# Optimization experiments

Measured on AMD Instinct MI355X. Metric: run time of the kernel, lower is better.

The kernel has to match this reference:

```python
import jax, jax.numpy as jnp
import numpy as np

N, DEG, F = 500000, 16, 128
H1, H2, OUT = 256, 256, 128


def setup_inputs() -> dict:
    key = jax.random.key(0)
    ks = jax.random.split(key, 8)
    s = lambda fan_in: 1.0 / np.sqrt(fan_in)
    return {
        "message": jax.random.normal(ks[0], (N, DEG, F), dtype=jnp.float32),
        "features": jax.random.normal(ks[1], (N, F), dtype=jnp.float32),
        "global_features": jax.random.normal(ks[2], (N, F), dtype=jnp.float32),
        "W1": jax.random.normal(ks[3], (3 * F, H1), dtype=jnp.float32) * s(3 * F),
        "b1": jnp.zeros((H1,), dtype=jnp.float32),
        "W2": jax.random.normal(ks[4], (H1, H2), dtype=jnp.float32) * s(H1),
        "b2": jnp.zeros((H2,), dtype=jnp.float32),
        "W3": jax.random.normal(ks[5], (H2, OUT), dtype=jnp.float32) * s(H2),
        "b3": jnp.zeros((OUT,), dtype=jnp.float32),
    }


def reference(message, features, global_features, W1, b1, W2, b2, W3, b3):
    # mailbox sum-aggregate over neighbors: [N, deg, F] -> [N, F]
    agg = jnp.sum(message, axis=1)
    # concat aggregated messages with node + global features: [N, 3F]
    x = jnp.concatenate([agg, features, global_features], axis=1)
    # MLP: Linear+ReLU, Linear+ReLU, Linear
    h = jax.nn.relu(x @ W1 + b1)
    h = jax.nn.relu(h @ W2 + b2)
    out = h @ W3 + b3
    # row-wise L2 (Frobenius over dim=1) normalization
    norm = jnp.linalg.norm(out, axis=1, keepdims=True)
    return out / (norm + 1e-8)
```

## Files before the change

### kernel.cpp

```cpp
#include <hip/hip_runtime.h>


typedef short short8   __attribute__((ext_vector_type(8)));
typedef short short4_t __attribute__((ext_vector_type(4)));
typedef float f32x4    __attribute__((ext_vector_type(4)));

#define SWZ(row, off) ((off) ^ (((row) & 7) << 4))

__device__ __forceinline__ unsigned short f2bf(float f) {
    unsigned int u = __float_as_uint(f);
    u += 0x7fffu + ((u >> 16) & 1u);
    return (unsigned short)(u >> 16);
}

__global__ void prep_weights(const float* __restrict__ W1,
                             const float* __restrict__ W2,
                             const float* __restrict__ W3,
                             short* __restrict__ pw1,
                             short* __restrict__ pw2,
                             short* __restrict__ pw3) {
    int idx = blockIdx.x * 256 + threadIdx.x;
    if (idx < 98304) {
        int j = idx & 7, l = (idx >> 3) & 63, g = idx >> 9;
        int ks = g % 12, tn = g / 12;
        int n = tn * 16 + (l & 15);
        int k = ks * 32 + ((l >> 4) << 3) + j;
        pw1[idx] = (short)f2bf(W1[k * 256 + n]);
    } else if (idx < 98304 + 65536) {
        int e = idx - 98304;
        int j = e & 7, l = (e >> 3) & 63, g = e >> 9;
        int ks = g & 7, tn = g >> 3;
        int n = tn * 16 + (l & 15);
        int k = ks * 32 + ((l >> 4) << 3) + j;
        pw2[e] = (short)f2bf(W2[k * 256 + n]);
    } else if (idx < 98304 + 65536 + 32768) {
        int e = idx - 98304 - 65536;
        int j = e & 7, l = (e >> 3) & 63, g = e >> 9;
        int ks = g & 7, tn = g >> 3;
        int n = tn * 16 + (l & 15);
        int k = ks * 32 + ((l >> 4) << 3) + j;
        pw3[e] = (short)f2bf(W3[k * 128 + n]);
    }
}

__global__ __launch_bounds__(256, 4) void node_net_fused(
    const float* __restrict__ msg,
    const float* __restrict__ feat,
    const float* __restrict__ glob,
    const float* __restrict__ b1v,
    const float* __restrict__ b2v,
    const float* __restrict__ b3v,
    const short* __restrict__ pw1,
    const short* __restrict__ pw2,
    const short* __restrict__ pw3,
    float* __restrict__ out,
    int n_rows)
{
    __shared__ char lds[32768];
    char* regA = lds;
    char* regB = lds + 16384;

    {
        const unsigned key = ((unsigned)blockIdx.x * 2654435761u) >> 30;
        const int spin = (int)key * 500;
        for (int i = 0; i < spin; ++i)
            asm volatile("s_nop 0" ::: "memory");
    }

    const int tid  = threadIdx.x;
    const int lane = tid & 63;
    const int w    = tid >> 6;
    const int lr   = lane & 15;
    const int lk   = lane >> 4;
    const long long r0 = (long long)blockIdx.x * 32;

    const f32x4 zero4 = {0.f, 0.f, 0.f, 0.f};

    f32x4 fr[4], gr[4];
    #pragma unroll
    for (int q = 0; q < 4; ++q) {
        int r = (tid >> 5) + q * 8;
        long long row = r0 + r;
        fr[q] = zero4; gr[q] = zero4;
        if (row < n_rows) {
            fr[q] = __builtin_nontemporal_load((const f32x4*)feat + row * 32 + (tid & 31));
            gr[q] = __builtin_nontemporal_load((const f32x4*)glob + row * 32 + (tid & 31));
        }
    }

    #pragma unroll 1
    for (int pp = 0; pp < 4; ++pp) {
        const int rA = 8 * w + 2 * pp;
        const long long rowA = r0 + rA;
        const f32x4* base = (const f32x4*)msg + rowA * 512;
        f32x4 tA[8], tB[8];
        const bool okA = rowA < n_rows;
        const bool okB = (rowA + 1) < n_rows;
        #pragma unroll
        for (int i = 0; i < 8; ++i)
            tA[i] = okA ? __builtin_nontemporal_load(base + i * 64 + lane) : zero4;
        #pragma unroll
        for (int i = 0; i < 8; ++i)
            tB[i] = okB ? __builtin_nontemporal_load(base + 512 + i * 64 + lane) : zero4;
        f32x4 sA = ((tA[0]+tA[1])+(tA[2]+tA[3])) + ((tA[4]+tA[5])+(tA[6]+tA[7]));
        f32x4 sB = ((tB[0]+tB[1])+(tB[2]+tB[3])) + ((tB[4]+tB[5])+(tB[6]+tB[7]));
        #pragma unroll
        for (int c = 0; c < 4; ++c) {
            sA[c] += __shfl_xor(sA[c], 32);
            sB[c] += __shfl_xor(sB[c], 32);
        }
        f32x4 s = (lane < 32) ? sA : sB;
        short4_t s4;
        s4[0] = (short)f2bf(s[0]); s4[1] = (short)f2bf(s[1]);
        s4[2] = (short)f2bf(s[2]); s4[3] = (short)f2bf(s[3]);
        const int orow = rA + (lane >> 5);
        *(short4_t*)(regB + SWZ(orow, orow * 256 + (lane & 31) * 8)) = s4;
    }
    __syncthreads();

    #pragma unroll
    for (int q = 0; q < 4; ++q) {
        int r = (tid >> 5) + q * 8;
        short4_t s4;
        s4[0] = (short)f2bf(fr[q][0]); s4[1] = (short)f2bf(fr[q][1]);
        s4[2] = (short)f2bf(fr[q][2]); s4[3] = (short)f2bf(fr[q][3]);
        *(short4_t*)(regA + SWZ(r, r * 256 + (tid & 31) * 8)) = s4;
    }

    f32x4 acc1[2][4];
    #pragma unroll
    for (int ri = 0; ri < 2; ++ri)
        #pragma unroll
        for (int ci = 0; ci < 4; ++ci) acc1[ri][ci] = zero4;

    #pragma unroll
    for (int s = 0; s < 4; ++s) {
        short8 a[2], b[4];
        #pragma unroll
        for (int ri = 0; ri < 2; ++ri) {
            int row = ri * 16 + lr;
            a[ri] = *(const short8*)(regB + SWZ(row, row * 256 + s * 64 + lk * 16));
        }
        #pragma unroll
        for (int ci = 0; ci < 4; ++ci) {
            int tn = w * 4 + ci;
            b[ci] = *(const short8*)(pw1 + (((tn * 12 + s) * 64 + lane) << 3));
        }
        #pragma unroll
        for (int ri = 0; ri < 2; ++ri)
            #pragma unroll
            for (int ci = 0; ci < 4; ++ci)
                acc1[ri][ci] = __builtin_amdgcn_mfma_f32_16x16x32_bf16(
                    a[ri], b[ci], acc1[ri][ci], 0, 0, 0);
    }
    __syncthreads();

    #pragma unroll
    for (int q = 0; q < 4; ++q) {
        int r = (tid >> 5) + q * 8;
        short4_t s4;
        s4[0] = (short)f2bf(gr[q][0]); s4[1] = (short)f2bf(gr[q][1]);
        s4[2] = (short)f2bf(gr[q][2]); s4[3] = (short)f2bf(gr[q][3]);
        *(short4_t*)(regB + 8192 + SWZ(r, r * 256 + (tid & 31) * 8)) = s4;
    }

    #pragma unroll
    for (int s = 0; s < 4; ++s) {
        short8 a[2], b[4];
        #pragma unroll
        for (int ri = 0; ri < 2; ++ri) {
            int row = ri * 16 + lr;
            a[ri] = *(const short8*)(regA + SWZ(row, row * 256 + s * 64 + lk * 16));
        }
        #pragma unroll
        for (int ci = 0; ci < 4; ++ci) {
            int tn = w * 4 + ci;
            b[ci] = *(const short8*)(pw1 + (((tn * 12 + 4 + s) * 64 + lane) << 3));
        }
        #pragma unroll
        for (int ri = 0; ri < 2; ++ri)
            #pragma unroll
            for (int ci = 0; ci < 4; ++ci)
                acc1[ri][ci] = __builtin_amdgcn_mfma_f32_16x16x32_bf16(
                    a[ri], b[ci], acc1[ri][ci], 0, 0, 0);
    }
    __syncthreads();

    #pragma unroll
    for (int s = 0; s < 4; ++s) {
        short8 a[2], b[4];
        #pragma unroll
        for (int ri = 0; ri < 2; ++ri) {
            int row = ri * 16 + lr;
            a[ri] = *(const short8*)(regB + 8192 + SWZ(row, row * 256 + s * 64 + lk * 16));
        }
        #pragma unroll
        for (int ci = 0; ci < 4; ++ci) {
            int tn = w * 4 + ci;
            b[ci] = *(const short8*)(pw1 + (((tn * 12 + 8 + s) * 64 + lane) << 3));
        }
        #pragma unroll
        for (int ri = 0; ri < 2; ++ri)
            #pragma unroll
            for (int ci = 0; ci < 4; ++ci)
                acc1[ri][ci] = __builtin_amdgcn_mfma_f32_16x16x32_bf16(
                    a[ri], b[ci], acc1[ri][ci], 0, 0, 0);
    }

    #pragma unroll
    for (int ci = 0; ci < 4; ++ci) {
        int col = w * 64 + ci * 16 + lr;
        float bias = b1v[col];
        #pragma unroll
        for (int ri = 0; ri < 2; ++ri)
            #pragma unroll
            for (int i = 0; i < 4; ++i) {
                int row = ri * 16 + lk * 4 + i;
                float v = fmaxf(acc1[ri][ci][i] + bias, 0.f);
                *(short*)(regA + SWZ(row, row * 512 + col * 2)) = (short)f2bf(v);
            }
    }
    __syncthreads();

    f32x4 acc2[2][4];
    #pragma unroll
    for (int ri = 0; ri < 2; ++ri)
        #pragma unroll
        for (int ci = 0; ci < 4; ++ci) acc2[ri][ci] = zero4;

    #pragma unroll
    for (int s = 0; s < 8; ++s) {
        short8 a[2], b[4];
        #pragma unroll
        for (int ri = 0; ri < 2; ++ri) {
            int row = ri * 16 + lr;
            a[ri] = *(const short8*)(regA + SWZ(row, row * 512 + s * 64 + lk * 16));
        }
        #pragma unroll
        for (int ci = 0; ci < 4; ++ci) {
            int tn = w * 4 + ci;
            b[ci] = *(const short8*)(pw2 + (((tn * 8 + s) * 64 + lane) << 3));
        }
        #pragma unroll
        for (int ri = 0; ri < 2; ++ri)
            #pragma unroll
            for (int ci = 0; ci < 4; ++ci)
                acc2[ri][ci] = __builtin_amdgcn_mfma_f32_16x16x32_bf16(
                    a[ri], b[ci], acc2[ri][ci], 0, 0, 0);
    }

    #pragma unroll
    for (int ci = 0; ci < 4; ++ci) {
        int col = w * 64 + ci * 16 + lr;
        float bias = b2v[col];
        #pragma unroll
        for (int ri = 0; ri < 2; ++ri)
            #pragma unroll
            for (int i = 0; i < 4; ++i) {
                int row = ri * 16 + lk * 4 + i;
                float v = fmaxf(acc2[ri][ci][i] + bias, 0.f);
                *(short*)(regB + SWZ(row, row * 512 + col * 2)) = (short)f2bf(v);
            }
    }
    __syncthreads();

    f32x4 acc3[2][2];
    #pragma unroll
    for (int ri = 0; ri < 2; ++ri)
        #pragma unroll
        for (int ci = 0; ci < 2; ++ci) acc3[ri][ci] = zero4;

    #pragma unroll
    for (int s = 0; s < 8; ++s) {
        short8 a[2], b[2];
        #pragma unroll
        for (int ri = 0; ri < 2; ++ri) {
            int row = ri * 16 + lr;
            a[ri] = *(const short8*)(regB + SWZ(row, row * 512 + s * 64 + lk * 16));
        }
        #pragma unroll
        for (int ci = 0; ci < 2; ++ci) {
            int tn = w * 2 + ci;
            b[ci] = *(const short8*)(pw3 + (((tn * 8 + s) * 64 + lane) << 3));
        }
        #pragma unroll
        for (int ri = 0; ri < 2; ++ri)
            #pragma unroll
            for (int ci = 0; ci < 2; ++ci)
                acc3[ri][ci] = __builtin_amdgcn_mfma_f32_16x16x32_bf16(
                    a[ri], b[ci], acc3[ri][ci], 0, 0, 0);
    }

    #pragma unroll
    for (int ci = 0; ci < 2; ++ci) {
        int col = w * 32 + ci * 16 + lr;
        float bias = b3v[col];
        #pragma unroll
        for (int ri = 0; ri < 2; ++ri)
            #pragma unroll
            for (int i = 0; i < 4; ++i) {
                int row = ri * 16 + lk * 4 + i;
                float v = acc3[ri][ci][i] + bias;
                *(float*)(regA + SWZ(row, row * 512 + col * 4)) = v;
            }
    }
    __syncthreads();

    #pragma unroll
    for (int pass = 0; pass < 4; ++pass) {
        const int r  = (tid >> 5) + pass * 8;
        const int fl = tid & 31;
        f32x4 v = *(const f32x4*)(regA + SWZ(r, r * 512 + fl * 16));
        float ss = v[0]*v[0] + v[1]*v[1] + v[2]*v[2] + v[3]*v[3];
        ss += __shfl_xor(ss, 1, 32);
        ss += __shfl_xor(ss, 2, 32);
        ss += __shfl_xor(ss, 4, 32);
        ss += __shfl_xor(ss, 8, 32);
        ss += __shfl_xor(ss, 16, 32);
        float inv = 1.f / (sqrtf(ss) + 1e-8f);
        long long row = r0 + r;
        if (row < n_rows) {
            f32x4 o = v * inv;
            __builtin_nontemporal_store(o, (f32x4*)out + row * 32 + fl);
        }
    }
}

extern "C" void kernel_launch(void* const* d_in, const int* in_sizes, int n_in,
                              void* d_out, int out_size, void* d_ws, size_t ws_size,
                              hipStream_t stream) {
    const float* msg  = (const float*)d_in[0];
    const float* feat = (const float*)d_in[1];
    const float* glob = (const float*)d_in[2];
    const float* W1   = (const float*)d_in[3];
    const float* b1   = (const float*)d_in[4];
    const float* W2   = (const float*)d_in[5];
    const float* b2   = (const float*)d_in[6];
    const float* W3   = (const float*)d_in[7];
    const float* b3   = (const float*)d_in[8];
    float* out = (float*)d_out;

    const int n_rows = in_sizes[1] / 128;

    short* pw1 = (short*)d_ws;
    short* pw2 = pw1 + 98304;
    short* pw3 = pw2 + 65536;

    hipLaunchKernelGGL(prep_weights, dim3(768), dim3(256), 0, stream,
                       W1, W2, W3, pw1, pw2, pw3);

    const int nblocks = (n_rows + 31) / 32;
    hipLaunchKernelGGL(node_net_fused, dim3(nblocks), dim3(256), 0, stream,
                       msg, feat, glob, b1, b2, b3, pw1, pw2, pw3, out, n_rows);
}
```

Measured before the change: 1.119 ms.

## Process two 32-row tiles per block, prefetching second tile's messages during MLP

Each block now handles 64 rows as two 32-row tiles. The message loads for the second tile are spread across the first tile's MLP stages in register buffers, so HBM reads overlap MFMA work. Feature and global inputs are staged into LDS together, so layer 1 runs as one 12-step K loop with fewer barriers. The staggered-start spin loop is removed. LDS grows to 48KB, launch bounds drop to 3 blocks per CU, and the extra prefetch registers raise register pressure.

```diff
diff --git a/kernel.cpp b/kernel.cpp
--- a/kernel.cpp
+++ b/kernel.cpp
@@ -43,7 +43,7 @@
     }
 }
 
-__global__ __launch_bounds__(256, 4) void node_net_fused(
+__global__ __launch_bounds__(256, 3) void node_net_fused2(
     const float* __restrict__ msg,
     const float* __restrict__ feat,
     const float* __restrict__ glob,
@@ -56,27 +56,48 @@
     float* __restrict__ out,
     int n_rows)
 {
-    __shared__ char lds[32768];
-    char* regA = lds;
-    char* regB = lds + 16384;
-
-    {
-        const unsigned key = ((unsigned)blockIdx.x * 2654435761u) >> 30;
-        const int spin = (int)key * 500;
-        for (int i = 0; i < spin; ++i)
-            asm volatile("s_nop 0" ::: "memory");
-    }
+    __shared__ char lds[49152];
+    char* XA = lds;
+    char* H  = lds + 24576;
+    char* AB = lds + 40960;
 
     const int tid  = threadIdx.x;
     const int lane = tid & 63;
     const int w    = tid >> 6;
     const int lr   = lane & 15;
     const int lk   = lane >> 4;
-    const long long r0 = (long long)blockIdx.x * 32;
-
+    const long long r0 = (long long)blockIdx.x * 64;
     const f32x4 zero4 = {0.f, 0.f, 0.f, 0.f};
 
     f32x4 fr[4], gr[4];
+    f32x4 cA[8], cB[8];
+
+#define ISSUE_PAIR(k) {                                                        \
+    const long long gA_ = r0 + 32 + 8 * w + 2 * (k);                           \
+    const f32x4* base_ = (const f32x4*)msg + gA_ * 512;                        \
+    const bool okA_ = gA_ < n_rows, okB_ = (gA_ + 1) < n_rows;                 \
+    _Pragma("unroll")                                                          \
+    for (int i = 0; i < 8; ++i)                                                \
+        cA[i] = okA_ ? __builtin_nontemporal_load(base_ + i * 64 + lane) : zero4; \
+    _Pragma("unroll")                                                          \
+    for (int i = 0; i < 8; ++i)                                                \
+        cB[i] = okB_ ? __builtin_nontemporal_load(base_ + 512 + i * 64 + lane) : zero4; }
+
+#define CONSUME_PAIR(k) {                                                      \
+    f32x4 sA_ = ((cA[0]+cA[1])+(cA[2]+cA[3])) + ((cA[4]+cA[5])+(cA[6]+cA[7])); \
+    f32x4 sB_ = ((cB[0]+cB[1])+(cB[2]+cB[3])) + ((cB[4]+cB[5])+(cB[6]+cB[7])); \
+    _Pragma("unroll")                                                          \
+    for (int c = 0; c < 4; ++c) {                                              \
+        sA_[c] += __shfl_xor(sA_[c], 32);                                      \
+        sB_[c] += __shfl_xor(sB_[c], 32);                                      \
+    }                                                                          \
+    f32x4 s_ = (lane < 32) ? sA_ : sB_;                                        \
+    short4_t s4_;                                                              \
+    s4_[0]=(short)f2bf(s_[0]); s4_[1]=(short)f2bf(s_[1]);                      \
+    s4_[2]=(short)f2bf(s_[2]); s4_[3]=(short)f2bf(s_[3]);                      \
+    const int rb_ = 8 * w + 2 * (k) + (lane >> 5);                             \
+    *(short4_t*)(AB + SWZ(rb_, rb_ * 256 + (lane & 31) * 8)) = s4_; }
+
     #pragma unroll
     for (int q = 0; q < 4; ++q) {
         int r = (tid >> 5) + q * 8;
@@ -111,41 +132,42 @@
         }
         f32x4 s = (lane < 32) ? sA : sB;
         short4_t s4;
-        s4[0] = (short)f2bf(s[0]); s4[1] = (short)f2bf(s[1]);
-        s4[2] = (short)f2bf(s[2]); s4[3] = (short)f2bf(s[3]);
+        s4[0]=(short)f2bf(s[0]); s4[1]=(short)f2bf(s[1]);
+        s4[2]=(short)f2bf(s[2]); s4[3]=(short)f2bf(s[3]);
         const int orow = rA + (lane >> 5);
-        *(short4_t*)(regB + SWZ(orow, orow * 256 + (lane & 31) * 8)) = s4;
-    }
-    __syncthreads();
-
+        *(short4_t*)(XA + SWZ(orow, orow * 256 + (lane & 31) * 8)) = s4;
+    }
     #pragma unroll
     for (int q = 0; q < 4; ++q) {
         int r = (tid >> 5) + q * 8;
-        short4_t s4;
-        s4[0] = (short)f2bf(fr[q][0]); s4[1] = (short)f2bf(fr[q][1]);
-        s4[2] = (short)f2bf(fr[q][2]); s4[3] = (short)f2bf(fr[q][3]);
-        *(short4_t*)(regA + SWZ(r, r * 256 + (tid & 31) * 8)) = s4;
-    }
-
+        short4_t sf, sg;
+        sf[0]=(short)f2bf(fr[q][0]); sf[1]=(short)f2bf(fr[q][1]);
+        sf[2]=(short)f2bf(fr[q][2]); sf[3]=(short)f2bf(fr[q][3]);
+        sg[0]=(short)f2bf(gr[q][0]); sg[1]=(short)f2bf(gr[q][1]);
+        sg[2]=(short)f2bf(gr[q][2]); sg[3]=(short)f2bf(gr[q][3]);
+        *(short4_t*)(XA + 8192  + SWZ(r, r * 256 + (tid & 31) * 8)) = sf;
+        *(short4_t*)(XA + 16384 + SWZ(r, r * 256 + (tid & 31) * 8)) = sg;
+    }
+    __syncthreads();
+
+    ISSUE_PAIR(0)
     f32x4 acc1[2][4];
     #pragma unroll
     for (int ri = 0; ri < 2; ++ri)
         #pragma unroll
         for (int ci = 0; ci < 4; ++ci) acc1[ri][ci] = zero4;
-
-    #pragma unroll
-    for (int s = 0; s < 4; ++s) {
+    #pragma unroll
+    for (int ks = 0; ks < 12; ++ks) {
+        const int p = ks >> 2, s = ks & 3;
         short8 a[2], b[4];
         #pragma unroll
         for (int ri = 0; ri < 2; ++ri) {
             int row = ri * 16 + lr;
-            a[ri] = *(const short8*)(regB + SWZ(row, row * 256 + s * 64 + lk * 16));
-        }
-        #pragma unroll
-        for (int ci = 0; ci < 4; ++ci) {
-            int tn = w * 4 + ci;
-            b[ci] = *(const short8*)(pw1 + (((tn * 12 + s) * 64 + lane) << 3));
-        }
+            a[ri] = *(const short8*)(XA + p * 8192 + SWZ(row, row * 256 + s * 64 + lk * 16));
+        }
+        #pragma unroll
+        for (int ci = 0; ci < 4; ++ci)
+            b[ci] = *(const short8*)(pw1 + ((((w * 4 + ci) * 12 + ks) * 64 + lane) << 3));
         #pragma unroll
         for (int ri = 0; ri < 2; ++ri)
             #pragma unroll
@@ -153,60 +175,6 @@
                 acc1[ri][ci] = __builtin_amdgcn_mfma_f32_16x16x32_bf16(
                     a[ri], b[ci], acc1[ri][ci], 0, 0, 0);
     }
-    __syncthreads();
-
-    #pragma unroll
-    for (int q = 0; q < 4; ++q) {
-        int r = (tid >> 5) + q * 8;
-        short4_t s4;
-        s4[0] = (short)f2bf(gr[q][0]); s4[1] = (short)f2bf(gr[q][1]);
-        s4[2] = (short)f2bf(gr[q][2]); s4[3] = (short)f2bf(gr[q][3]);
-        *(short4_t*)(regB + 8192 + SWZ(r, r * 256 + (tid & 31) * 8)) = s4;
-    }
-
-    #pragma unroll
-    for (int s = 0; s < 4; ++s) {
-        short8 a[2], b[4];
-        #pragma unroll
-        for (int ri = 0; ri < 2; ++ri) {
-            int row = ri * 16 + lr;
-            a[ri] = *(const short8*)(regA + SWZ(row, row * 256 + s * 64 + lk * 16));
-        }
-        #pragma unroll
-        for (int ci = 0; ci < 4; ++ci) {
-            int tn = w * 4 + ci;
-            b[ci] = *(const short8*)(pw1 + (((tn * 12 + 4 + s) * 64 + lane) << 3));
-        }
-        #pragma unroll
-        for (int ri = 0; ri < 2; ++ri)
-            #pragma unroll
-            for (int ci = 0; ci < 4; ++ci)
-                acc1[ri][ci] = __builtin_amdgcn_mfma_f32_16x16x32_bf16(
-                    a[ri], b[ci], acc1[ri][ci], 0, 0, 0);
-    }
-    __syncthreads();
-
-    #pragma unroll
-    for (int s = 0; s < 4; ++s) {
-        short8 a[2], b[4];
-        #pragma unroll
-        for (int ri = 0; ri < 2; ++ri) {
-            int row = ri * 16 + lr;
-            a[ri] = *(const short8*)(regB + 8192 + SWZ(row, row * 256 + s * 64 + lk * 16));
-        }
-        #pragma unroll
-        for (int ci = 0; ci < 4; ++ci) {
-            int tn = w * 4 + ci;
-            b[ci] = *(const short8*)(pw1 + (((tn * 12 + 8 + s) * 64 + lane) << 3));
-        }
-        #pragma unroll
-        for (int ri = 0; ri < 2; ++ri)
-            #pragma unroll
-            for (int ci = 0; ci < 4; ++ci)
-                acc1[ri][ci] = __builtin_amdgcn_mfma_f32_16x16x32_bf16(
-                    a[ri], b[ci], acc1[ri][ci], 0, 0, 0);
-    }
-
     #pragma unroll
     for (int ci = 0; ci < 4; ++ci) {
         int col = w * 64 + ci * 16 + lr;
@@ -217,100 +185,112 @@
             for (int i = 0; i < 4; ++i) {
                 int row = ri * 16 + lk * 4 + i;
                 float v = fmaxf(acc1[ri][ci][i] + bias, 0.f);
-                *(short*)(regA + SWZ(row, row * 512 + col * 2)) = (short)f2bf(v);
-            }
-    }
-    __syncthreads();
-
-    f32x4 acc2[2][4];
-    #pragma unroll
-    for (int ri = 0; ri < 2; ++ri)
-        #pragma unroll
-        for (int ci = 0; ci < 4; ++ci) acc2[ri][ci] = zero4;
-
-    #pragma unroll
-    for (int s = 0; s < 8; ++s) {
-        short8 a[2], b[4];
-        #pragma unroll
-        for (int ri = 0; ri < 2; ++ri) {
-            int row = ri * 16 + lr;
-            a[ri] = *(const short8*)(regA + SWZ(row, row * 512 + s * 64 + lk * 16));
+                *(short*)(H + SWZ(row, row * 512 + col * 2)) = (short)f2bf(v);
+            }
+    }
+    __syncthreads();
+
+    CONSUME_PAIR(0)
+    ISSUE_PAIR(1)
+    {
+        f32x4 acc2[2][4];
+        #pragma unroll
+        for (int ri = 0; ri < 2; ++ri)
+            #pragma unroll
+            for (int ci = 0; ci < 4; ++ci) acc2[ri][ci] = zero4;
+        #pragma unroll
+        for (int s = 0; s < 8; ++s) {
+            short8 a[2], b[4];
+            #pragma unroll
+            for (int ri = 0; ri < 2; ++ri) {
+                int row = ri * 16 + lr;
+                a[ri] = *(const short8*)(H + SWZ(row, row * 512 + s * 64 + lk * 16));
+            }
+            #pragma unroll
+            for (int ci = 0; ci < 4; ++ci)
+                b[ci] = *(const short8*)(pw2 + ((((w * 4 + ci) * 8 + s) * 64 + lane) << 3));
+            #pragma unroll
+            for (int ri = 0; ri < 2; ++ri)
+                #pragma unroll
+                for (int ci = 0; ci < 4; ++ci)
+                    acc2[ri][ci] = __builtin_amdgcn_mfma_f32_16x16x32_bf16(
+                        a[ri], b[ci], acc2[ri][ci], 0, 0, 0);
         }
         #pragma unroll
         for (int ci = 0; ci < 4; ++ci) {
-            int tn = w * 4 + ci;
-            b[ci] = *(const short8*)(pw2 + (((tn * 8 + s) * 64 + lane) << 3));
-        }
-        #pragma unroll
-        for (int ri = 0; ri < 2; ++ri)
-            #pragma unroll
-            for (int ci = 0; ci < 4; ++ci)
-                acc2[ri][ci] = __builtin_amdgcn_mfma_f32_16x16x32_bf16(
-                    a[ri], b[ci], acc2[ri][ci], 0, 0, 0);
-    }
-
-    #pragma unroll
-    for (int ci = 0; ci < 4; ++ci) {
-        int col = w * 64 + ci * 16 + lr;
-        float bias = b2v[col];
-        #pragma unroll
-        for (int ri = 0; ri < 2; ++ri)
-            #pragma unroll
-            for (int i = 0; i < 4; ++i) {
-                int row = ri * 16 + lk * 4 + i;
-                float v = fmaxf(acc2[ri][ci][i] + bias, 0.f);
-                *(short*)(regB + SWZ(row, row * 512 + col * 2)) = (short)f2bf(v);
-            }
-    }
-    __syncthreads();
-
-    f32x4 acc3[2][2];
-    #pragma unroll
-    for (int ri = 0; ri < 2; ++ri)
-        #pragma unroll
-        for (int ci = 0; ci < 2; ++ci) acc3[ri][ci] = zero4;
-
-    #pragma unroll
-    for (int s = 0; s < 8; ++s) {
-        short8 a[2], b[2];
-        #pragma unroll
-        for (int ri = 0; ri < 2; ++ri) {
-            int row = ri * 16 + lr;
-            a[ri] = *(const short8*)(regB + SWZ(row, row * 512 + s * 64 + lk * 16));
+            int col = w * 64 + ci * 16 + lr;
+            float bias = b2v[col];
+            #pragma unroll
+            for (int ri = 0; ri < 2; ++ri)
+                #pragma unroll
+                for (int i = 0; i < 4; ++i) {
+                    int row = ri * 16 + lk * 4 + i;
+                    float v = fmaxf(acc2[ri][ci][i] + bias, 0.f);
+                    *(short*)(XA + SWZ(row, row * 512 + col * 2)) = (short)f2bf(v);
+                }
+        }
+    }
+    __syncthreads();
+
+    CONSUME_PAIR(1)
+    ISSUE_PAIR(2)
+    {
+        f32x4 acc3[2][2];
+        #pragma unroll
+        for (int ri = 0; ri < 2; ++ri)
+            #pragma unroll
+            for (int ci = 0; ci < 2; ++ci) acc3[ri][ci] = zero4;
+        #pragma unroll
+        for (int s = 0; s < 8; ++s) {
+            short8 a[2], b[2];
+            #pragma unroll
+            for (int ri = 0; ri < 2; ++ri) {
+                int row = ri * 16 + lr;
+                a[ri] = *(const short8*)(XA + SWZ(row, row * 512 + s * 64 + lk * 16));
+            }
+            #pragma unroll
+            for (int ci = 0; ci < 2; ++ci)
+                b[ci] = *(const short8*)(pw3 + ((((w * 2 + ci) * 8 + s) * 64 + lane) << 3));
+            #pragma unroll
+            for (int ri = 0; ri < 2; ++ri)
+                #pragma unroll
+                for (int ci = 0; ci < 2; ++ci)
+                    acc3[ri][ci] = __builtin_amdgcn_mfma_f32_16x16x32_bf16(
+                        a[ri], b[ci], acc3[ri][ci], 0, 0, 0);
         }
         #pragma unroll
         for (int ci = 0; ci < 2; ++ci) {
-            int tn = w * 2 + ci;
-            b[ci] = *(const short8*)(pw3 + (((tn * 8 + s) * 64 + lane) << 3));
-        }
-        #pragma unroll
-        for (int ri = 0; ri < 2; ++ri)
-            #pragma unroll
-            for (int ci = 0; ci < 2; ++ci)
-                acc3[ri][ci] = __builtin_amdgcn_mfma_f32_16x16x32_bf16(
-                    a[ri], b[ci], acc3[ri][ci], 0, 0, 0);
-    }
-
-    #pragma unroll
-    for (int ci = 0; ci < 2; ++ci) {
-        int col = w * 32 + ci * 16 + lr;
-        float bias = b3v[col];
-        #pragma unroll
-        for (int ri = 0; ri < 2; ++ri)
-            #pragma unroll
-            for (int i = 0; i < 4; ++i) {
-                int row = ri * 16 + lk * 4 + i;
-                float v = acc3[ri][ci][i] + bias;
-                *(float*)(regA + SWZ(row, row * 512 + col * 4)) = v;
-            }
-    }
-    __syncthreads();
-
+            int col = w * 32 + ci * 16 + lr;
+            float bias = b3v[col];
+            #pragma unroll
+            for (int ri = 0; ri < 2; ++ri)
+                #pragma unroll
+                for (int i = 0; i < 4; ++i) {
+                    int row = ri * 16 + lk * 4 + i;
+                    float v = acc3[ri][ci][i] + bias;
+                    *(float*)(H + SWZ(row, row * 512 + col * 4)) = v;
+                }
+        }
+    }
+    __syncthreads();
+
+    CONSUME_PAIR(2)
+    ISSUE_PAIR(3)
+    #pragma unroll
+    for (int q = 0; q < 4; ++q) {
+        int r = (tid >> 5) + q * 8;
+        long long row = r0 + 32 + r;
+        fr[q] = zero4; gr[q] = zero4;
+        if (row < n_rows) {
+            fr[q] = __builtin_nontemporal_load((const f32x4*)feat + row * 32 + (tid & 31));
+            gr[q] = __builtin_nontemporal_load((const f32x4*)glob + row * 32 + (tid & 31));
+        }
+    }
     #pragma unroll
     for (int pass = 0; pass < 4; ++pass) {
         const int r  = (tid >> 5) + pass * 8;
         const int fl = tid & 31;
-        f32x4 v = *(const f32x4*)(regA + SWZ(r, r * 512 + fl * 16));
+        f32x4 v = *(const f32x4*)(H + SWZ(r, r * 512 + fl * 16));
         float ss = v[0]*v[0] + v[1]*v[1] + v[2]*v[2] + v[3]*v[3];
         ss += __shfl_xor(ss, 1, 32);
         ss += __shfl_xor(ss, 2, 32);
@@ -324,6 +304,161 @@
             __builtin_nontemporal_store(o, (f32x4*)out + row * 32 + fl);
         }
     }
+    __syncthreads();
+
+    CONSUME_PAIR(3)
+    #pragma unroll
+    for (int q = 0; q < 4; ++q) {
+        int r = (tid >> 5) + q * 8;
+        short4_t sf, sg;
+        sf[0]=(short)f2bf(fr[q][0]); sf[1]=(short)f2bf(fr[q][1]);
+        sf[2]=(short)f2bf(fr[q][2]); sf[3]=(short)f2bf(fr[q][3]);
+        sg[0]=(short)f2bf(gr[q][0]); sg[1]=(short)f2bf(gr[q][1]);
+        sg[2]=(short)f2bf(gr[q][2]); sg[3]=(short)f2bf(gr[q][3]);
+        *(short4_t*)(XA + 8192  + SWZ(r, r * 256 + (tid & 31) * 8)) = sf;
+        *(short4_t*)(XA + 16384 + SWZ(r, r * 256 + (tid & 31) * 8)) = sg;
+    }
+    __syncthreads();
+
+    #pragma unroll
+    for (int ri = 0; ri < 2; ++ri)
+        #pragma unroll
+        for (int ci = 0; ci < 4; ++ci) acc1[ri][ci] = zero4;
+    #pragma unroll
+    for (int ks = 0; ks < 12; ++ks) {
+        const int p = ks >> 2, s = ks & 3;
+        const char* abase = (p == 0) ? AB : (XA + p * 8192);
+        short8 a[2], b[4];
+        #pragma unroll
+        for (int ri = 0; ri < 2; ++ri) {
+            int row = ri * 16 + lr;
+            a[ri] = *(const short8*)(abase + SWZ(row, row * 256 + s * 64 + lk * 16));
+        }
+        #pragma unroll
+        for (int ci = 0; ci < 4; ++ci)
+            b[ci] = *(const short8*)(pw1 + ((((w * 4 + ci) * 12 + ks) * 64 + lane) << 3));
+        #pragma unroll
+        for (int ri = 0; ri < 2; ++ri)
+            #pragma unroll
+            for (int ci = 0; ci < 4; ++ci)
+                acc1[ri][ci] = __builtin_amdgcn_mfma_f32_16x16x32_bf16(
+                    a[ri], b[ci], acc1[ri][ci], 0, 0, 0);
+    }
+    #pragma unroll
+    for (int ci = 0; ci < 4; ++ci) {
+        int col = w * 64 + ci * 16 + lr;
+        float bias = b1v[col];
+        #pragma unroll
+        for (int ri = 0; ri < 2; ++ri)
+            #pragma unroll
+            for (int i = 0; i < 4; ++i) {
+                int row = ri * 16 + lk * 4 + i;
+                float v = fmaxf(acc1[ri][ci][i] + bias, 0.f);
+                *(short*)(H + SWZ(row, row * 512 + col * 2)) = (short)f2bf(v);
+            }
+    }
+    __syncthreads();
+
+    {
+        f32x4 acc2[2][4];
+        #pragma unroll
+        for (int ri = 0; ri < 2; ++ri)
+            #pragma unroll
+            for (int ci = 0; ci < 4; ++ci) acc2[ri][ci] = zero4;
+        #pragma unroll
+        for (int s = 0; s < 8; ++s) {
+            short8 a[2], b[4];
+            #pragma unroll
+            for (int ri = 0; ri < 2; ++ri) {
+                int row = ri * 16 + lr;
+                a[ri] = *(const short8*)(H + SWZ(row, row * 512 + s * 64 + lk * 16));
+            }
+            #pragma unroll
+            for (int ci = 0; ci < 4; ++ci)
+                b[ci] = *(const short8*)(pw2 + ((((w * 4 + ci) * 8 + s) * 64 + lane) << 3));
+            #pragma unroll
+            for (int ri = 0; ri < 2; ++ri)
+                #pragma unroll
+                for (int ci = 0; ci < 4; ++ci)
+                    acc2[ri][ci] = __builtin_amdgcn_mfma_f32_16x16x32_bf16(
+                        a[ri], b[ci], acc2[ri][ci], 0, 0, 0);
+        }
+        #pragma unroll
+        for (int ci = 0; ci < 4; ++ci) {
+            int col = w * 64 + ci * 16 + lr;
+            float bias = b2v[col];
+            #pragma unroll
+            for (int ri = 0; ri < 2; ++ri)
+                #pragma unroll
+                for (int i = 0; i < 4; ++i) {
+                    int row = ri * 16 + lk * 4 + i;
+                    float v = fmaxf(acc2[ri][ci][i] + bias, 0.f);
+                    *(short*)(XA + SWZ(row, row * 512 + col * 2)) = (short)f2bf(v);
+                }
+        }
+    }
+    __syncthreads();
+
+    {
+        f32x4 acc3[2][2];
+        #pragma unroll
+        for (int ri = 0; ri < 2; ++ri)
+            #pragma unroll
+            for (int ci = 0; ci < 2; ++ci) acc3[ri][ci] = zero4;
+        #pragma unroll
+        for (int s = 0; s < 8; ++s) {
+            short8 a[2], b[2];
+            #pragma unroll
+            for (int ri = 0; ri < 2; ++ri) {
+                int row = ri * 16 + lr;
+                a[ri] = *(const short8*)(XA + SWZ(row, row * 512 + s * 64 + lk * 16));
+            }
+            #pragma unroll
+            for (int ci = 0; ci < 2; ++ci)
+                b[ci] = *(const short8*)(pw3 + ((((w * 2 + ci) * 8 + s) * 64 + lane) << 3));
+            #pragma unroll
+            for (int ri = 0; ri < 2; ++ri)
+                #pragma unroll
+                for (int ci = 0; ci < 2; ++ci)
+                    acc3[ri][ci] = __builtin_amdgcn_mfma_f32_16x16x32_bf16(
+                        a[ri], b[ci], acc3[ri][ci], 0, 0, 0);
+        }
+        #pragma unroll
+        for (int ci = 0; ci < 2; ++ci) {
+            int col = w * 32 + ci * 16 + lr;
+            float bias = b3v[col];
+            #pragma unroll
+            for (int ri = 0; ri < 2; ++ri)
+                #pragma unroll
+                for (int i = 0; i < 4; ++i) {
+                    int row = ri * 16 + lk * 4 + i;
+                    float v = acc3[ri][ci][i] + bias;
+                    *(float*)(H + SWZ(row, row * 512 + col * 4)) = v;
+                }
+        }
+    }
+    __syncthreads();
+
+    #pragma unroll
+    for (int pass = 0; pass < 4; ++pass) {
+        const int r  = (tid >> 5) + pass * 8;
+        const int fl = tid & 31;
+        f32x4 v = *(const f32x4*)(H + SWZ(r, r * 512 + fl * 16));
+        float ss = v[0]*v[0] + v[1]*v[1] + v[2]*v[2] + v[3]*v[3];
+        ss += __shfl_xor(ss, 1, 32);
+        ss += __shfl_xor(ss, 2, 32);
+        ss += __shfl_xor(ss, 4, 32);
+        ss += __shfl_xor(ss, 8, 32);
+        ss += __shfl_xor(ss, 16, 32);
+        float inv = 1.f / (sqrtf(ss) + 1e-8f);
+        long long row = r0 + 32 + r;
+        if (row < n_rows) {
+            f32x4 o = v * inv;
+            __builtin_nontemporal_store(o, (f32x4*)out + row * 32 + fl);
+        }
+    }
+#undef ISSUE_PAIR
+#undef CONSUME_PAIR
 }
 
 extern "C" void kernel_launch(void* const* d_in, const int* in_sizes, int n_in,
@@ -349,7 +484,7 @@
     hipLaunchKernelGGL(prep_weights, dim3(768), dim3(256), 0, stream,
                        W1, W2, W3, pw1, pw2, pw3);
 
-    const int nblocks = (n_rows + 31) / 32;
-    hipLaunchKernelGGL(node_net_fused, dim3(nblocks), dim3(256), 0, stream,
+    const int nblocks = (n_rows + 63) / 64;
+    hipLaunchKernelGGL(node_net_fused2, dim3(nblocks), dim3(256), 0, stream,
                        msg, feat, glob, b1, b2, b3, pw1, pw2, pw3, out, n_rows);
 }
```

Result: slower. 1.812 ms (+62.0%).
